# Optimization experiments

Measured on AMD Instinct MI355X. Metric: run time of the kernel, lower is better.

Reference implementation:

```python
import jax, jax.numpy as jnp
import numpy as np

B, S, F_IN, F_OUT = 8, 128, 768, 768
NUM_REL = 41           # num_dependencies + 1
NUM_LAYER = 2
N_HEAD, HID = 8, 96    # hidden_dim = embed_dim // n_head
EMB = 768


def setup_inputs() -> dict:
    key = jax.random.key(0)
    ks = jax.random.split(key, 14)
    s = 1.0 / np.sqrt(F_IN)
    inp = {
        "x": jax.random.normal(ks[0], (B, S, F_IN), dtype=jnp.float32),
        "adj": jax.random.uniform(ks[1], (B, NUM_REL, S, S), dtype=jnp.float32),
        "q": jax.random.normal(ks[2], (B, EMB), dtype=jnp.float32),
        # R-GCN params (stacked over layers)
        "w_rgcn": jax.random.uniform(ks[3], (NUM_LAYER, NUM_REL, F_IN, F_OUT), minval=-s, maxval=s),
        "score_w": jax.random.uniform(ks[4], (NUM_LAYER, F_OUT), minval=-s, maxval=s),
        "score_b": jax.random.uniform(ks[5], (NUM_LAYER,), minval=-s, maxval=s),
        # Attention params (stored as [in, out] for x @ W)
        "wk": jax.random.uniform(ks[6], (EMB, N_HEAD * HID), minval=-s, maxval=s),
        "bk": jnp.zeros((N_HEAD * HID,), jnp.float32),
        "wq": jax.random.uniform(ks[7], (EMB, N_HEAD * HID), minval=-s, maxval=s),
        "bq": jnp.zeros((N_HEAD * HID,), jnp.float32),
        "wbil": jax.random.uniform(ks[8], (HID, HID), minval=-1.0 / np.sqrt(HID), maxval=1.0 / np.sqrt(HID)),
        "wproj": jax.random.uniform(ks[9], (N_HEAD * HID, EMB), minval=-s, maxval=s),
        "bproj": jnp.zeros((EMB,), jnp.float32),
    }
    return inp


def _rgcn_layer(h, adj, w, sw, sb):
    # h: [B,S,I]; adj: [B,R,S,S]; w: [R,I,O]
    hidden = jnp.einsum("bsi,rio->brso", h, w)            # per-relation transform
    denom = jnp.sum(adj, axis=3, keepdims=True)           # [B,R,S,1]
    intm = jnp.einsum("brsk,brko->brso", adj, hidden)     # relation-wise aggregation
    div = intm / jnp.where(denom == 0, jnp.ones_like(denom), denom)
    logits = jnp.einsum("brso,o->brs", div, sw) + sb      # score Linear(out->1)
    r_coeffs = jax.nn.softmax(logits, axis=1)             # softmax over relations
    out = jnp.einsum("brso,brs->bso", div, r_coeffs)
    return jax.nn.relu(out)


def _attention(k, q, wk, bk, wq, bq, wbil, wproj, bproj):
    # k: [B,S,E]; q: [B,E] -> [B,1,E]
    q3 = q[:, None, :]
    kx = (k @ wk + bk).reshape(B, S, N_HEAD, HID)
    qx = (q3 @ wq + bq).reshape(B, 1, N_HEAD, HID)
    qw = jnp.einsum("bqhd,de->bqhe", qx, wbil)            # bi_linear score
    score = jnp.einsum("bqhe,bkhe->bhqk", qw, kx)
    attn = jax.nn.softmax(score, axis=-1)
    o = jnp.einsum("bhqk,bkhd->bqhd", attn, kx).reshape(B, 1, N_HEAD * HID)
    return o @ wproj + bproj                              # [B,1,EMB]


def reference(x, adj, q, w_rgcn, score_w, score_b, wk, bk, wq, bq, wbil, wproj, bproj):
    h = x
    for l in range(NUM_LAYER):
        h = _rgcn_layer(h, adj, w_rgcn[l], score_w[l], score_b[l])
    return _attention(h, q, wk, bk, wq, bq, wbil, wproj, bproj)
```

## Files before the change

kernel.cpp:

```cpp
#include <hip/hip_runtime.h>
#include <stdint.h>

#define B_ 8
#define S_ 128
#define R_ 41
#define F_ 768
#define NH_ 8
#define HID_ 96
#define BS_ (B_*S_)
#define SM_SCALE 256.0f
#define NG_ 21

typedef _Float16 f16;
typedef _Float16 f16x8 __attribute__((ext_vector_type(8)));
typedef _Float16 f16x4 __attribute__((ext_vector_type(4)));
typedef _Float16 f16x2 __attribute__((ext_vector_type(2)));
typedef float f32x4 __attribute__((ext_vector_type(4)));
typedef float f32x2 __attribute__((ext_vector_type(2)));

#define GLD16(gp, lp) __builtin_amdgcn_global_load_lds((const __attribute__((address_space(1))) uint32_t*)(gp), (__attribute__((address_space(3))) uint32_t*)(lp), 16, 0, 0)

__device__ __forceinline__ float wredsum(float v){
  #pragma unroll
  for (int o=32;o;o>>=1) v += __shfl_down(v,o,64);
  return v;
}

__global__ __launch_bounds__(256) void kConvWV(const float* __restrict__ w, const float* __restrict__ sw,
                                               f16* __restrict__ wT, float* __restrict__ v) {
  int bid = blockIdx.x;
  int it = bid % 12, r = bid / 12;
  __shared__ float t[64*68];
  int tid = threadIdx.x;
  int ri = tid >> 2, c = tid & 3;
  float vacc = 0.f;
  for (int ot = 0; ot < 12; ++ot) {
    const float* src = w + ((size_t)r*F_ + (it*64 + ri))*F_ + ot*64 + c*16;
    const float* swp = sw + ot*64 + c*16;
    __syncthreads();
    #pragma unroll
    for (int j=0;j<4;j++){
      f32x4 v4 = *(const f32x4*)(src + j*4);
      f32x4 s4 = *(const f32x4*)(swp + j*4);
      vacc += v4.x*s4.x + v4.y*s4.y + v4.z*s4.z + v4.w*s4.w;
      *(f32x4*)&t[ri*68 + c*16 + j*4] = v4;
    }
    __syncthreads();
    int ro = tid >> 2;
    f16 outv[16];
    #pragma unroll
    for (int j=0;j<16;j++) outv[j] = (f16)t[(c*16+j)*68 + ro];
    f16* dst = wT + ((size_t)r*F_ + (ot*64+ro))*F_ + it*64 + c*16;
    *(f16x8*)dst = *(f16x8*)&outv[0];
    *(f16x8*)(dst+8) = *(f16x8*)&outv[8];
  }
  vacc += __shfl_down(vacc, 1, 64);
  vacc += __shfl_down(vacc, 2, 64);
  if (c == 0) v[(size_t)r*F_ + it*64 + ri] = vacc;
}

__global__ __launch_bounds__(256) void kConvW(const float* __restrict__ w, f16* __restrict__ wT) {
  int bid = blockIdx.x;
  int ot = bid % 12; int it = (bid/12) % 12; int r = bid / 144;
  __shared__ float t[64*68];
  int tid = threadIdx.x;
  int ri = tid >> 2, c = tid & 3;
  const float* src = w + ((size_t)r*F_ + (it*64 + ri))*F_ + ot*64 + c*16;
  #pragma unroll
  for (int j=0;j<4;j++){
    f32x4 v4 = *(const f32x4*)(src + j*4);
    *(f32x4*)&t[ri*68 + c*16 + j*4] = v4;
  }
  __syncthreads();
  int ro = tid >> 2;
  f16 outv[16];
  #pragma unroll
  for (int j=0;j<16;j++) outv[j] = (f16)t[(c*16+j)*68 + ro];
  f16* dst = wT + ((size_t)r*F_ + (ot*64+ro))*F_ + it*64 + c*16;
  *(f16x8*)dst = *(f16x8*)&outv[0];
  *(f16x8*)(dst+8) = *(f16x8*)&outv[8];
}

template<typename T>
__global__ __launch_bounds__(256) void kTransTo16T(const T* __restrict__ h, f16* __restrict__ hT) {
  int bid = blockIdx.x;
  int st = bid & 1; int ft = (bid>>1) % 12; int b = bid / 24;
  __shared__ f16 t[64*72];
  int tid = threadIdx.x;
  int sl = tid>>2, c = tid&3;
  const T* src = h + ((size_t)b*S_ + st*64 + sl)*F_ + ft*64 + c*16;
  f16 tmp[16];
  #pragma unroll
  for (int j=0;j<16;j++) tmp[j] = (f16)src[j];
  *(f16x8*)&t[sl*72 + c*16]     = *(f16x8*)&tmp[0];
  *(f16x8*)&t[sl*72 + c*16 + 8] = *(f16x8*)&tmp[8];
  __syncthreads();
  int fl = tid>>2;
  f16 outv[16];
  #pragma unroll
  for (int j=0;j<16;j++) outv[j] = t[(c*16+j)*72 + fl];
  f16* dst = hT + ((size_t)b*F_ + ft*64 + fl)*S_ + st*64 + c*16;
  *(f16x8*)dst = *(f16x8*)&outv[0];
  *(f16x8*)(dst+8) = *(f16x8*)&outv[8];
}

__global__ __launch_bounds__(256) void kUL(const float* __restrict__ h, const float* __restrict__ v,
                    const float* __restrict__ adj, const float* __restrict__ sb_all, int l,
                    float* __restrict__ dinv, float* __restrict__ lg) {
  int bid = blockIdx.x;
  int r = bid % R_, b = bid / R_;
  __shared__ float v_s[F_];
  __shared__ float u_s[S_];
  int tid = threadIdx.x;
  #pragma unroll
  for (int j=0;j<3;j++) v_s[tid + j*256] = v[(size_t)r*F_ + tid + j*256];
  __syncthreads();
  int wid = tid>>6, lane = tid&63;
  for (int kl=0; kl<32; ++kl){
    int k = wid*32 + kl;
    const float* hr = h + ((size_t)b*S_ + k)*F_ + lane*12;
    const float* vp = &v_s[lane*12];
    float acc=0.f;
    #pragma unroll
    for (int j=0;j<3;j++){
      f32x4 a = *(const f32x4*)(hr+j*4);
      f32x4 c4 = *(const f32x4*)(vp+j*4);
      acc += a.x*c4.x+a.y*c4.y+a.z*c4.z+a.w*c4.w;
    }
    acc = wredsum(acc);
    if (lane==0) u_s[k] = acc;
  }
  __syncthreads();
  int s = tid>>1, half = tid&1;
  const float* arow = adj + ((size_t)bid*S_ + s)*S_ + half*64;
  const float* up = &u_s[half*64];
  float ssum=0.f, sdot=0.f;
  #pragma unroll
  for (int j=0;j<16;j++){
    f32x4 a = *(const f32x4*)(arow + j*4);
    ssum += a.x+a.y+a.z+a.w;
    sdot += a.x*up[j*4] + a.y*up[j*4+1] + a.z*up[j*4+2] + a.w*up[j*4+3];
  }
  ssum += __shfl_xor(ssum,1,64);
  sdot += __shfl_xor(sdot,1,64);
  if (half==0){
    float dv = (ssum==0.0f)?1.0f:(1.0f/ssum);
    dinv[(size_t)bid*S_ + s] = dv;
    lg[(size_t)bid*S_ + s] = sdot*dv + sb_all[l];
  }
}

__global__ __launch_bounds__(64) void kSM16(const float* __restrict__ lg, const float* __restrict__ dinv,
                     const float* __restrict__ adj, f16* __restrict__ M) {
  int bid = blockIdx.x;
  int b = bid >> 7, s = bid & 127;
  int lane = threadIdx.x;
  __shared__ float coef[R_];
  float x = (lane < R_) ? lg[((size_t)b*R_ + lane)*S_ + s] : -1e30f;
  float m = x;
  #pragma unroll
  for (int o=32;o;o>>=1) m = fmaxf(m, __shfl_xor(m,o,64));
  float e = (lane < R_) ? expf(x - m) : 0.f;
  float sum = e;
  #pragma unroll
  for (int o=32;o;o>>=1) sum += __shfl_xor(sum,o,64);
  if (lane < R_) coef[lane] = e/sum * SM_SCALE * dinv[((size_t)b*R_ + lane)*S_ + s];
  __syncthreads();
  for (int r=0;r<R_;r++){
    float cc = coef[r];
    size_t base = (((size_t)(b*R_+r))*S_ + s)*S_ + lane*2;
    f32x2 a2 = *(const f32x2*)(adj + base);
    f16x2 o2; o2[0]=(f16)(a2.x*cc); o2[1]=(f16)(a2.y*cc);
    *(f16x2*)(M + base) = o2;
  }
}

__global__ __launch_bounds__(256) void kGgemm(const f16* __restrict__ M, const f16* __restrict__ hT, f16* __restrict__ G) {
  __shared__ f16 lds[2*16384];
  f16* lsA = lds;
  f16* lsB = lds + 16384;
  int bid = blockIdx.x;
  int nt = bid % 6; int r = (bid/6) % R_; int b = bid/(6*R_);
  int tid = threadIdx.x, wid = tid>>6, lane = tid&63;
  const f16* Ab = M + (size_t)(b*R_ + r)*(S_*S_);
  const f16* Bb = hT + ((size_t)b*F_ + nt*128)*S_;
  #pragma unroll
  for (int j=0;j<8;j++){
    int qd = wid*8 + j;
    GLD16(Ab + qd*512 + lane*8, lsA + qd*512);
    GLD16(Bb + qd*512 + lane*8, lsB + qd*512);
  }
  __syncthreads();
  f32x4 acc[4][4] = {};
  int wr = wid>>1, wc = wid&1;
  int lr = lane&15, kk0 = (lane>>4)*8;
  #pragma unroll
  for (int ks=0;ks<4;ks++){
    int kk = ks*32 + kk0;
    f16x8 av[4], bv[4];
    #pragma unroll
    for (int i=0;i<4;i++) av[i] = *(const f16x8*)&lsA[(wr*64+i*16+lr)*128 + kk];
    #pragma unroll
    for (int i=0;i<4;i++) bv[i] = *(const f16x8*)&lsB[(wc*64+i*16+lr)*128 + kk];
    #pragma unroll
    for (int mi=0;mi<4;mi++)
      #pragma unroll
      for (int ni=0;ni<4;ni++)
        acc[mi][ni] = __builtin_amdgcn_mfma_f32_16x16x32_f16(av[mi],bv[ni],acc[mi][ni],0,0,0);
  }
  __syncthreads();
  #pragma unroll
  for (int mi=0;mi<4;mi++)
    #pragma unroll
    for (int ni=0;ni<4;ni++){
      int row = wr*64 + mi*16 + (lane>>4)*4;
      int col = wc*64 + ni*16 + lr;
      #pragma unroll
      for (int i=0;i<4;i++)
        lds[(row+i)*136 + col] = (f16)acc[mi][ni][i];
    }
  __syncthreads();
  int row = tid>>1, seg = tid&1;
  f16* dst = G + ((size_t)(b*R_ + r)*S_ + row)*F_ + nt*128 + seg*64;
  const f16* sl = lds + row*136 + seg*64;
  #pragma unroll
  for (int j=0;j<8;j++) *(f16x8*)(dst + j*8) = *(const f16x8*)(sl + j*8);
}

__global__ __launch_bounds__(512,2) void kOutGemm(const f16* __restrict__ G, const f16* __restrict__ WT, float* __restrict__ Cp) {
  __shared__ f16 ls[2][2][256*64];
  int bid = blockIdx.x;
  int t12 = bid % 12, g = bid / 12;
  int nt = t12 % 3, mt = t12 / 3;
  int r0 = (g<20)? 2*g : 40;
  int nr = (g<20)? 2 : 1;
  int tid = threadIdx.x, wid = tid>>6, lane = tid&63;
  size_t abase[4], bbase[4];
  #pragma unroll
  for (int j=0;j<4;j++){
    int chunk = wid*4 + j;
    int arow = mt*256 + chunk*8 + (lane>>3);
    int b = arow >> 7, s = arow & 127;
    abase[j] = ((size_t)b*R_*S_ + s)*(size_t)F_ + (lane&7)*8;
    int orow = nt*256 + chunk*8 + (lane>>3);
    bbase[j] = (size_t)orow*F_ + (lane&7)*8;
  }
  f32x4 acc[8][4] = {};
  int wr = wid>>2, wc = wid&3;
  int lr = lane&15, kk0 = (lane>>4)*8;
  int nsteps = nr*12;
  auto STAGE = [&](int bf, int step){
    int r = r0 + step/12, it = step%12;
    const f16* Ar = G  + (size_t)r*S_*F_;
    const f16* Br = WT + (size_t)r*F_*F_;
    #pragma unroll
    for (int j=0;j<4;j++){
      int chunk = wid*4 + j;
      GLD16(Ar + abase[j] + it*64, &ls[bf][0][chunk*512]);
      GLD16(Br + bbase[j] + it*64, &ls[bf][1][chunk*512]);
    }
  };
  STAGE(0, 0);
  __syncthreads();
  int cur = 0;
  for (int step=0; step<nsteps; ++step){
    if (step+1 < nsteps) STAGE(cur^1, step+1);
    __builtin_amdgcn_s_setprio(1);
    #pragma unroll
    for (int ks=0;ks<2;ks++){
      int kk = ks*32 + kk0;
      f16x8 av[8], bv[4];
      #pragma unroll
      for (int i=0;i<8;i++) av[i] = *(const f16x8*)&ls[cur][0][(wr*128+i*16+lr)*64 + kk];
      #pragma unroll
      for (int i=0;i<4;i++) bv[i] = *(const f16x8*)&ls[cur][1][(wc*64+i*16+lr)*64 + kk];
      #pragma unroll
      for (int mi=0;mi<8;mi++)
        #pragma unroll
        for (int ni=0;ni<4;ni++)
          acc[mi][ni] = __builtin_amdgcn_mfma_f32_16x16x32_f16(av[mi],bv[ni],acc[mi][ni],0,0,0);
    }
    __builtin_amdgcn_s_setprio(0);
    __syncthreads();
    cur ^= 1;
  }
  #pragma unroll
  for (int mi=0;mi<8;mi++)
    #pragma unroll
    for (int ni=0;ni<4;ni++){
      int row = mt*256 + wr*128 + mi*16 + (lane>>4)*4;
      int col = nt*256 + wc*64 + ni*16 + lr;
      #pragma unroll
      for (int i=0;i<4;i++)
        Cp[((size_t)g*BS_ + row + i)*F_ + col] = acc[mi][ni][i];
    }
}

__global__ __launch_bounds__(256) void kReduce(const float* __restrict__ Cp, float* __restrict__ h32, f16* __restrict__ h16o) {
  int t = blockIdx.x*256 + threadIdx.x;
  size_t i4 = (size_t)t*4;
  f32x4 s = {};
  #pragma unroll
  for (int g=0; g<NG_; g++){
    f32x4 v4 = *(const f32x4*)(Cp + (size_t)g*BS_*F_ + i4);
    s.x += v4.x; s.y += v4.y; s.z += v4.z; s.w += v4.w;
  }
  const float inv = 1.0f/SM_SCALE;
  f32x4 rr;
  rr.x = fmaxf(s.x*inv, 0.f); rr.y = fmaxf(s.y*inv, 0.f);
  rr.z = fmaxf(s.z*inv, 0.f); rr.w = fmaxf(s.w*inv, 0.f);
  *(f32x4*)(h32 + i4) = rr;
  f16x4 o; o[0]=(f16)rr.x; o[1]=(f16)rr.y; o[2]=(f16)rr.z; o[3]=(f16)rr.w;
  *(f16x4*)(h16o + i4) = o;
}

__global__ __launch_bounds__(256) void kKx(const f16* __restrict__ A, const f16* __restrict__ BT,
                    const float* __restrict__ bias, float* __restrict__ C) {
  __shared__ f16 ls[2][2][128*64];
  int bid = blockIdx.x;
  int nt = bid % 6, mt = bid / 6;
  int tid = threadIdx.x, wid = tid>>6, lane = tid&63;
  size_t abase[4], bbase[4];
  #pragma unroll
  for (int j=0;j<4;j++){
    int qd = wid*4 + j;
    int row = mt*128 + qd*8 + (lane>>3);
    abase[j] = (size_t)row*F_ + (lane&7)*8;
    int o = nt*128 + qd*8 + (lane>>3);
    bbase[j] = (size_t)o*F_ + (lane&7)*8;
  }
  f32x4 acc[4][4] = {};
  int wr = wid>>1, wc = wid&1;
  int lr = lane&15, kk0 = (lane>>4)*8;
  auto STAGE = [&](int bf, int it){
    #pragma unroll
    for (int j=0;j<4;j++){
      int qd = wid*4+j;
      GLD16(A + abase[j] + it*64, &ls[bf][0][qd*512]);
      GLD16(BT + bbase[j] + it*64, &ls[bf][1][qd*512]);
    }
  };
  STAGE(0, 0);
  __syncthreads();
  int cur = 0;
  for (int it=0; it<12; ++it){
    if (it+1 < 12) STAGE(cur^1, it+1);
    #pragma unroll
    for (int ks=0;ks<2;ks++){
      int kk = ks*32 + kk0;
      f16x8 av[4], bv[4];
      #pragma unroll
      for (int i=0;i<4;i++) av[i] = *(const f16x8*)&ls[cur][0][(wr*64+i*16+lr)*64 + kk];
      #pragma unroll
      for (int i=0;i<4;i++) bv[i] = *(const f16x8*)&ls[cur][1][(wc*64+i*16+lr)*64 + kk];
      #pragma unroll
      for (int mi=0;mi<4;mi++)
        #pragma unroll
        for (int ni=0;ni<4;ni++)
          acc[mi][ni] = __builtin_amdgcn_mfma_f32_16x16x32_f16(av[mi],bv[ni],acc[mi][ni],0,0,0);
    }
    __syncthreads();
    cur ^= 1;
  }
  #pragma unroll
  for (int mi=0;mi<4;mi++)
    #pragma unroll
    for (int ni=0;ni<4;ni++){
      int row = mt*128 + wr*64 + mi*16 + (lane>>4)*4;
      int col = nt*128 + wc*64 + ni*16 + lr;
      float bb = bias[col];
      #pragma unroll
      for (int i=0;i<4;i++)
        C[(size_t)(row+i)*F_ + col] = acc[mi][ni][i] + bb;
    }
}

__global__ __launch_bounds__(256) void kAttn(const float* __restrict__ kx, const float* __restrict__ qin,
                      const float* __restrict__ wq, const float* __restrict__ bq,
                      const float* __restrict__ wbil, float* __restrict__ obuf) {
  int bid = blockIdx.x; int h = bid & 7; int b = bid >> 3;
  __shared__ float qx[HID_], qw[HID_], sc[S_];
  __shared__ float smax, ssum;
  int t = threadIdx.x;
  if (t < HID_) {
    float a0=0.f,a1=0.f,a2=0.f,a3=0.f;
    const float* qp = qin + (size_t)b*F_;
    const float* wp = wq + h*HID_ + t;
    for (int i=0;i<F_;i+=4){
      a0 += qp[i]*wp[(size_t)i*F_];
      a1 += qp[i+1]*wp[(size_t)(i+1)*F_];
      a2 += qp[i+2]*wp[(size_t)(i+2)*F_];
      a3 += qp[i+3]*wp[(size_t)(i+3)*F_];
    }
    qx[t] = a0+a1+a2+a3 + bq[h*HID_+t];
  }
  __syncthreads();
  if (t < HID_) {
    float a0=0.f,a1=0.f;
    for (int e=0;e<HID_;e+=2){ a0 += qx[e]*wbil[e*HID_+t]; a1 += qx[e+1]*wbil[(e+1)*HID_+t]; }
    qw[t] = a0+a1;
  }
  __syncthreads();
  if (t < S_) {
    float a0=0.f,a1=0.f;
    const float* kp = kx + ((size_t)b*S_ + t)*F_ + h*HID_;
    for (int e=0;e<HID_;e+=2){ a0 += qw[e]*kp[e]; a1 += qw[e+1]*kp[e+1]; }
    sc[t] = a0+a1;
  }
  __syncthreads();
  if (t < 64) {
    float m = fmaxf(sc[t], sc[t+64]);
    #pragma unroll
    for (int o=32;o;o>>=1) m = fmaxf(m, __shfl_down(m,o,64));
    if (t==0) smax = m;
  }
  __syncthreads();
  if (t < S_) sc[t] = expf(sc[t]-smax);
  __syncthreads();
  if (t < 64) {
    float s = sc[t] + sc[t+64];
    s = wredsum(s);
    if (t==0) ssum = s;
  }
  __syncthreads();
  if (t < HID_) {
    float a0=0.f,a1=0.f;
    const float* kp = kx + ((size_t)b*S_)*F_ + h*HID_ + t;
    for (int k=0;k<S_;k+=2){ a0 += sc[k]*kp[(size_t)k*F_]; a1 += sc[k+1]*kp[(size_t)(k+1)*F_]; }
    obuf[(size_t)b*F_ + h*HID_ + t] = (a0+a1)/ssum;
  }
}

__global__ __launch_bounds__(256) void kProj(const float* __restrict__ obuf, const float* __restrict__ wproj,
                      const float* __restrict__ bproj, float* __restrict__ outp) {
  int bid = blockIdx.x; int b = bid/3, seg = bid%3;
  int t = threadIdx.x;
  __shared__ float ov[F_];
  for (int j=t;j<F_;j+=256) ov[j] = obuf[(size_t)b*F_ + j];
  __syncthreads();
  int col = seg*256 + t;
  float a0=0.f,a1=0.f,a2=0.f,a3=0.f;
  for (int j=0;j<F_;j+=4){
    a0 += ov[j]*wproj[(size_t)j*F_+col];
    a1 += ov[j+1]*wproj[(size_t)(j+1)*F_+col];
    a2 += ov[j+2]*wproj[(size_t)(j+2)*F_+col];
    a3 += ov[j+3]*wproj[(size_t)(j+3)*F_+col];
  }
  outp[(size_t)b*F_ + col] = bproj[col] + a0+a1+a2+a3;
}

extern "C" void kernel_launch(void* const* d_in, const int* in_sizes, int n_in,
                              void* d_out, int out_size, void* d_ws, size_t ws_size,
                              hipStream_t stream) {
  (void)in_sizes; (void)n_in; (void)out_size;
  const float* x      = (const float*)d_in[0];
  const float* adj    = (const float*)d_in[1];
  const float* qin    = (const float*)d_in[2];
  const float* w_rgcn = (const float*)d_in[3];
  const float* score_w= (const float*)d_in[4];
  const float* score_b= (const float*)d_in[5];
  const float* wk     = (const float*)d_in[6];
  const float* bk     = (const float*)d_in[7];
  const float* wq     = (const float*)d_in[8];
  const float* bq     = (const float*)d_in[9];
  const float* wbil   = (const float*)d_in[10];
  const float* wproj  = (const float*)d_in[11];
  const float* bproj  = (const float*)d_in[12];
  float* outp = (float*)d_out;

  char* p = (char*)d_ws;
  auto alloc = [&](size_t bytes)->char* {
    char* r = p; p += (bytes + 255) & ~(size_t)255; return r;
  };
  f16*   w16T  = (f16*)  alloc((size_t)R_*F_*F_*2);
  f16*   G16   = (f16*)  alloc((size_t)B_*R_*S_*F_*2);
  f16*   M16   = (f16*)  alloc((size_t)B_*R_*S_*S_*2);
  float* Cpart = (float*)alloc((size_t)NG_*BS_*F_*4);
  float* h32a  = (float*)alloc((size_t)BS_*F_*4);
  float* h32b  = (float*)alloc((size_t)BS_*F_*4);
  f16*   h16row= (f16*)  alloc((size_t)BS_*F_*2);
  f16*   h16T  = (f16*)  alloc((size_t)BS_*F_*2);
  float* kx    = (float*)alloc((size_t)BS_*F_*4);
  f16*   wkT   = (f16*)  alloc((size_t)F_*F_*2);
  float* vbuf  = (float*)alloc((size_t)R_*F_*4);
  float* dinv  = (float*)alloc((size_t)B_*R_*S_*4);
  float* lgb   = (float*)alloc((size_t)B_*R_*S_*4);
  float* obuf  = (float*)alloc((size_t)B_*F_*4);
  if ((size_t)(p - (char*)d_ws) > ws_size) return;

  const size_t WL = (size_t)R_*F_*F_;

  kConvWV<<<R_*12, 256, 0, stream>>>(w_rgcn, score_w, w16T, vbuf);
  kTransTo16T<float><<<192, 256, 0, stream>>>(x, h16T);
  kUL<<<B_*R_, 256, 0, stream>>>(x, vbuf, adj, score_b, 0, dinv, lgb);
  kSM16<<<B_*S_, 64, 0, stream>>>(lgb, dinv, adj, M16);
  kGgemm<<<B_*R_*6, 256, 0, stream>>>(M16, h16T, G16);
  kOutGemm<<<12*NG_, 512, 0, stream>>>(G16, w16T, Cpart);
  kReduce<<<768, 256, 0, stream>>>(Cpart, h32a, h16row);
  kTransTo16T<f16><<<192, 256, 0, stream>>>(h16row, h16T);

  kConvWV<<<R_*12, 256, 0, stream>>>(w_rgcn + WL, score_w + F_, w16T, vbuf);
  kUL<<<B_*R_, 256, 0, stream>>>(h32a, vbuf, adj, score_b, 1, dinv, lgb);
  kSM16<<<B_*S_, 64, 0, stream>>>(lgb, dinv, adj, M16);
  kGgemm<<<B_*R_*6, 256, 0, stream>>>(M16, h16T, G16);
  kOutGemm<<<12*NG_, 512, 0, stream>>>(G16, w16T, Cpart);
  kReduce<<<768, 256, 0, stream>>>(Cpart, h32b, h16row);

  kConvW<<<144, 256, 0, stream>>>(wk, wkT);
  kKx<<<48, 256, 0, stream>>>(h16row, wkT, bk, kx);
  kAttn<<<64, 256, 0, stream>>>(kx, qin, wq, bq, wbil, obuf);
  kProj<<<24, 256, 0, stream>>>(obuf, wproj, bproj, outp);
}
```

Before: 483.6 us.

## Swizzle LDS layouts in GEMMs and fuse reduce with transpose and weight conversion

Applies an XOR swizzle to the LDS tile layouts in kGgemm, kOutGemm and kKx so the MFMA operand reads avoid bank conflicts. It also fuses the partial-sum reduction with the f16 transpose into a new kReduceT kernel. The wk conversion is folded into the first kConvWV launch as extra blocks. Together these cut kernel launches and an extra pass over h, but the reduction now runs on 192 blocks instead of 768, which may lower memory parallelism. The final reduce also writes an unused transposed copy.

```diff
diff --git a/kernel.cpp b/kernel.cpp
--- a/kernel.cpp
+++ b/kernel.cpp
@@ -27,11 +27,33 @@
 }
 
 __global__ __launch_bounds__(256) void kConvWV(const float* __restrict__ w, const float* __restrict__ sw,
-                                               f16* __restrict__ wT, float* __restrict__ v) {
-  int bid = blockIdx.x;
+                                               f16* __restrict__ wT, float* __restrict__ v,
+                                               const float* __restrict__ wk, f16* __restrict__ wkT, int nwv) {
+  int bid = blockIdx.x;
+  int tid = threadIdx.x;
+  if (bid >= nwv) {
+    int b2 = bid - nwv;
+    int ot = b2 % 12; int it = b2 / 12;
+    __shared__ float t2[64*68];
+    int ri = tid >> 2, c = tid & 3;
+    const float* src = wk + (size_t)(it*64 + ri)*F_ + ot*64 + c*16;
+    #pragma unroll
+    for (int j=0;j<4;j++){
+      f32x4 v4 = *(const f32x4*)(src + j*4);
+      *(f32x4*)&t2[ri*68 + c*16 + j*4] = v4;
+    }
+    __syncthreads();
+    int ro = tid >> 2;
+    f16 outv[16];
+    #pragma unroll
+    for (int j=0;j<16;j++) outv[j] = (f16)t2[(c*16+j)*68 + ro];
+    f16* dst = wkT + (size_t)(ot*64+ro)*F_ + it*64 + c*16;
+    *(f16x8*)dst = *(f16x8*)&outv[0];
+    *(f16x8*)(dst+8) = *(f16x8*)&outv[8];
+    return;
+  }
   int it = bid % 12, r = bid / 12;
   __shared__ float t[64*68];
-  int tid = threadIdx.x;
   int ri = tid >> 2, c = tid & 3;
   float vacc = 0.f;
   for (int ot = 0; ot < 12; ++ot) {
@@ -59,36 +81,13 @@
   if (c == 0) v[(size_t)r*F_ + it*64 + ri] = vacc;
 }
 
-__global__ __launch_bounds__(256) void kConvW(const float* __restrict__ w, f16* __restrict__ wT) {
-  int bid = blockIdx.x;
-  int ot = bid % 12; int it = (bid/12) % 12; int r = bid / 144;
-  __shared__ float t[64*68];
-  int tid = threadIdx.x;
-  int ri = tid >> 2, c = tid & 3;
-  const float* src = w + ((size_t)r*F_ + (it*64 + ri))*F_ + ot*64 + c*16;
-  #pragma unroll
-  for (int j=0;j<4;j++){
-    f32x4 v4 = *(const f32x4*)(src + j*4);
-    *(f32x4*)&t[ri*68 + c*16 + j*4] = v4;
-  }
-  __syncthreads();
-  int ro = tid >> 2;
-  f16 outv[16];
-  #pragma unroll
-  for (int j=0;j<16;j++) outv[j] = (f16)t[(c*16+j)*68 + ro];
-  f16* dst = wT + ((size_t)r*F_ + (ot*64+ro))*F_ + it*64 + c*16;
-  *(f16x8*)dst = *(f16x8*)&outv[0];
-  *(f16x8*)(dst+8) = *(f16x8*)&outv[8];
-}
-
-template<typename T>
-__global__ __launch_bounds__(256) void kTransTo16T(const T* __restrict__ h, f16* __restrict__ hT) {
+__global__ __launch_bounds__(256) void kTransTo16T(const float* __restrict__ h, f16* __restrict__ hT) {
   int bid = blockIdx.x;
   int st = bid & 1; int ft = (bid>>1) % 12; int b = bid / 24;
   __shared__ f16 t[64*72];
   int tid = threadIdx.x;
   int sl = tid>>2, c = tid&3;
-  const T* src = h + ((size_t)b*S_ + st*64 + sl)*F_ + ft*64 + c*16;
+  const float* src = h + ((size_t)b*S_ + st*64 + sl)*F_ + ft*64 + c*16;
   f16 tmp[16];
   #pragma unroll
   for (int j=0;j<16;j++) tmp[j] = (f16)src[j];
@@ -187,21 +186,24 @@
   #pragma unroll
   for (int j=0;j<8;j++){
     int qd = wid*8 + j;
-    GLD16(Ab + qd*512 + lane*8, lsA + qd*512);
-    GLD16(Bb + qd*512 + lane*8, lsB + qd*512);
+    int rowg = qd*4 + (lane>>4);
+    int slotp = (lane&15) ^ ((j&3)*4 + (lane>>4));
+    GLD16(Ab + (size_t)rowg*128 + slotp*8, lsA + qd*512);
+    GLD16(Bb + (size_t)rowg*128 + slotp*8, lsB + qd*512);
   }
   __syncthreads();
   f32x4 acc[4][4] = {};
   int wr = wid>>1, wc = wid&1;
-  int lr = lane&15, kk0 = (lane>>4)*8;
+  int lr = lane&15, g4 = lane>>4;
   #pragma unroll
   for (int ks=0;ks<4;ks++){
-    int kk = ks*32 + kk0;
     f16x8 av[4], bv[4];
-    #pragma unroll
-    for (int i=0;i<4;i++) av[i] = *(const f16x8*)&lsA[(wr*64+i*16+lr)*128 + kk];
-    #pragma unroll
-    for (int i=0;i<4;i++) bv[i] = *(const f16x8*)&lsB[(wc*64+i*16+lr)*128 + kk];
+    int slotl = ks*4 + g4;
+    int slotp = slotl ^ lr;
+    #pragma unroll
+    for (int i=0;i<4;i++) av[i] = *(const f16x8*)&lsA[(wr*64+i*16+lr)*128 + slotp*8];
+    #pragma unroll
+    for (int i=0;i<4;i++) bv[i] = *(const f16x8*)&lsB[(wc*64+i*16+lr)*128 + slotp*8];
     #pragma unroll
     for (int mi=0;mi<4;mi++)
       #pragma unroll
@@ -235,19 +237,20 @@
   int r0 = (g<20)? 2*g : 40;
   int nr = (g<20)? 2 : 1;
   int tid = threadIdx.x, wid = tid>>6, lane = tid&63;
+  int swslot = (lane&7) ^ ((lane>>3)&7);
   size_t abase[4], bbase[4];
   #pragma unroll
   for (int j=0;j<4;j++){
     int chunk = wid*4 + j;
     int arow = mt*256 + chunk*8 + (lane>>3);
     int b = arow >> 7, s = arow & 127;
-    abase[j] = ((size_t)b*R_*S_ + s)*(size_t)F_ + (lane&7)*8;
+    abase[j] = ((size_t)b*R_*S_ + s)*(size_t)F_ + swslot*8;
     int orow = nt*256 + chunk*8 + (lane>>3);
-    bbase[j] = (size_t)orow*F_ + (lane&7)*8;
+    bbase[j] = (size_t)orow*F_ + swslot*8;
   }
   f32x4 acc[8][4] = {};
   int wr = wid>>2, wc = wid&3;
-  int lr = lane&15, kk0 = (lane>>4)*8;
+  int lr = lane&15, g4 = lane>>4, r7 = lane&7;
   int nsteps = nr*12;
   auto STAGE = [&](int bf, int step){
     int r = r0 + step/12, it = step%12;
@@ -268,12 +271,12 @@
     __builtin_amdgcn_s_setprio(1);
     #pragma unroll
     for (int ks=0;ks<2;ks++){
-      int kk = ks*32 + kk0;
+      int slotp = ((ks*4 + g4) ^ r7) * 8;
       f16x8 av[8], bv[4];
       #pragma unroll
-      for (int i=0;i<8;i++) av[i] = *(const f16x8*)&ls[cur][0][(wr*128+i*16+lr)*64 + kk];
-      #pragma unroll
-      for (int i=0;i<4;i++) bv[i] = *(const f16x8*)&ls[cur][1][(wc*64+i*16+lr)*64 + kk];
+      for (int i=0;i<8;i++) av[i] = *(const f16x8*)&ls[cur][0][(wr*128+i*16+lr)*64 + slotp];
+      #pragma unroll
+      for (int i=0;i<4;i++) bv[i] = *(const f16x8*)&ls[cur][1][(wc*64+i*16+lr)*64 + slotp];
       #pragma unroll
       for (int mi=0;mi<8;mi++)
         #pragma unroll
@@ -296,22 +299,42 @@
     }
 }
 
-__global__ __launch_bounds__(256) void kReduce(const float* __restrict__ Cp, float* __restrict__ h32, f16* __restrict__ h16o) {
-  int t = blockIdx.x*256 + threadIdx.x;
-  size_t i4 = (size_t)t*4;
-  f32x4 s = {};
-  #pragma unroll
-  for (int g=0; g<NG_; g++){
-    f32x4 v4 = *(const f32x4*)(Cp + (size_t)g*BS_*F_ + i4);
-    s.x += v4.x; s.y += v4.y; s.z += v4.z; s.w += v4.w;
-  }
+__global__ __launch_bounds__(256) void kReduceT(const float* __restrict__ Cp, float* __restrict__ h32,
+                                                f16* __restrict__ h16o, f16* __restrict__ hT) {
+  int bid = blockIdx.x;
+  int st = bid & 1; int ft = (bid>>1) % 12; int b = bid / 24;
+  __shared__ f16 t[64*72];
+  int tid = threadIdx.x;
+  int sl = tid>>2, c = tid&3;
+  size_t base = ((size_t)(b*S_ + st*64 + sl))*F_ + ft*64 + c*16;
   const float inv = 1.0f/SM_SCALE;
-  f32x4 rr;
-  rr.x = fmaxf(s.x*inv, 0.f); rr.y = fmaxf(s.y*inv, 0.f);
-  rr.z = fmaxf(s.z*inv, 0.f); rr.w = fmaxf(s.w*inv, 0.f);
-  *(f32x4*)(h32 + i4) = rr;
-  f16x4 o; o[0]=(f16)rr.x; o[1]=(f16)rr.y; o[2]=(f16)rr.z; o[3]=(f16)rr.w;
-  *(f16x4*)(h16o + i4) = o;
+  f16 tmp[16];
+  #pragma unroll
+  for (int q=0;q<4;q++){
+    f32x4 s4 = {};
+    #pragma unroll
+    for (int g=0; g<NG_; g++){
+      f32x4 v4 = *(const f32x4*)(Cp + (size_t)g*BS_*F_ + base + q*4);
+      s4.x += v4.x; s4.y += v4.y; s4.z += v4.z; s4.w += v4.w;
+    }
+    f32x4 rr;
+    rr.x = fmaxf(s4.x*inv, 0.f); rr.y = fmaxf(s4.y*inv, 0.f);
+    rr.z = fmaxf(s4.z*inv, 0.f); rr.w = fmaxf(s4.w*inv, 0.f);
+    *(f32x4*)(h32 + base + q*4) = rr;
+    tmp[q*4+0]=(f16)rr.x; tmp[q*4+1]=(f16)rr.y; tmp[q*4+2]=(f16)rr.z; tmp[q*4+3]=(f16)rr.w;
+  }
+  *(f16x8*)&t[sl*72 + c*16]     = *(f16x8*)&tmp[0];
+  *(f16x8*)&t[sl*72 + c*16 + 8] = *(f16x8*)&tmp[8];
+  *(f16x8*)(h16o + base)     = *(f16x8*)&tmp[0];
+  *(f16x8*)(h16o + base + 8) = *(f16x8*)&tmp[8];
+  __syncthreads();
+  int fl = tid>>2;
+  f16 outv[16];
+  #pragma unroll
+  for (int j=0;j<16;j++) outv[j] = t[(c*16+j)*72 + fl];
+  f16* dst = hT + ((size_t)b*F_ + ft*64 + fl)*S_ + st*64 + c*16;
+  *(f16x8*)dst = *(f16x8*)&outv[0];
+  *(f16x8*)(dst+8) = *(f16x8*)&outv[8];
 }
 
 __global__ __launch_bounds__(256) void kKx(const f16* __restrict__ A, const f16* __restrict__ BT,
@@ -320,18 +343,19 @@
   int bid = blockIdx.x;
   int nt = bid % 6, mt = bid / 6;
   int tid = threadIdx.x, wid = tid>>6, lane = tid&63;
+  int swslot = (lane&7) ^ ((lane>>3)&7);
   size_t abase[4], bbase[4];
   #pragma unroll
   for (int j=0;j<4;j++){
     int qd = wid*4 + j;
     int row = mt*128 + qd*8 + (lane>>3);
-    abase[j] = (size_t)row*F_ + (lane&7)*8;
+    abase[j] = (size_t)row*F_ + swslot*8;
     int o = nt*128 + qd*8 + (lane>>3);
-    bbase[j] = (size_t)o*F_ + (lane&7)*8;
+    bbase[j] = (size_t)o*F_ + swslot*8;
   }
   f32x4 acc[4][4] = {};
   int wr = wid>>1, wc = wid&1;
-  int lr = lane&15, kk0 = (lane>>4)*8;
+  int lr = lane&15, g4 = lane>>4, r7 = lane&7;
   auto STAGE = [&](int bf, int it){
     #pragma unroll
     for (int j=0;j<4;j++){
@@ -347,12 +371,12 @@
     if (it+1 < 12) STAGE(cur^1, it+1);
     #pragma unroll
     for (int ks=0;ks<2;ks++){
-      int kk = ks*32 + kk0;
+      int slotp = ((ks*4 + g4) ^ r7) * 8;
       f16x8 av[4], bv[4];
       #pragma unroll
-      for (int i=0;i<4;i++) av[i] = *(const f16x8*)&ls[cur][0][(wr*64+i*16+lr)*64 + kk];
-      #pragma unroll
-      for (int i=0;i<4;i++) bv[i] = *(const f16x8*)&ls[cur][1][(wc*64+i*16+lr)*64 + kk];
+      for (int i=0;i<4;i++) av[i] = *(const f16x8*)&ls[cur][0][(wr*64+i*16+lr)*64 + slotp];
+      #pragma unroll
+      for (int i=0;i<4;i++) bv[i] = *(const f16x8*)&ls[cur][1][(wc*64+i*16+lr)*64 + slotp];
       #pragma unroll
       for (int mi=0;mi<4;mi++)
         #pragma unroll
@@ -490,23 +514,21 @@
 
   const size_t WL = (size_t)R_*F_*F_;
 
-  kConvWV<<<R_*12, 256, 0, stream>>>(w_rgcn, score_w, w16T, vbuf);
-  kTransTo16T<float><<<192, 256, 0, stream>>>(x, h16T);
+  kConvWV<<<R_*12 + 144, 256, 0, stream>>>(w_rgcn, score_w, w16T, vbuf, wk, wkT, R_*12);
+  kTransTo16T<<<192, 256, 0, stream>>>(x, h16T);
   kUL<<<B_*R_, 256, 0, stream>>>(x, vbuf, adj, score_b, 0, dinv, lgb);
   kSM16<<<B_*S_, 64, 0, stream>>>(lgb, dinv, adj, M16);
   kGgemm<<<B_*R_*6, 256, 0, stream>>>(M16, h16T, G16);
   kOutGemm<<<12*NG_, 512, 0, stream>>>(G16, w16T, Cpart);
-  kReduce<<<768, 256, 0, stream>>>(Cpart, h32a, h16row);
-  kTransTo16T<f16><<<192, 256, 0, stream>>>(h16row, h16T);
-
-  kConvWV<<<R_*12, 256, 0, stream>>>(w_rgcn + WL, score_w + F_, w16T, vbuf);
+  kReduceT<<<192, 256, 0, stream>>>(Cpart, h32a, h16row, h16T);
+
+  kConvWV<<<R_*12, 256, 0, stream>>>(w_rgcn + WL, score_w + F_, w16T, vbuf, wk, wkT, R_*12);
   kUL<<<B_*R_, 256, 0, stream>>>(h32a, vbuf, adj, score_b, 1, dinv, lgb);
   kSM16<<<B_*S_, 64, 0, stream>>>(lgb, dinv, adj, M16);
   kGgemm<<<B_*R_*6, 256, 0, stream>>>(M16, h16T, G16);
   kOutGemm<<<12*NG_, 512, 0, stream>>>(G16, w16T, Cpart);
-  kReduce<<<768, 256, 0, stream>>>(Cpart, h32b, h16row);
-
-  kConvW<<<144, 256, 0, stream>>>(wk, wkT);
+  kReduceT<<<192, 256, 0, stream>>>(Cpart, h32b, h16row, h16T);
+
   kKx<<<48, 256, 0, stream>>>(h16row, wkT, bk, kx);
   kAttn<<<64, 256, 0, stream>>>(kx, qin, wq, bq, wbil, obuf);
   kProj<<<24, 256, 0, stream>>>(obuf, wproj, bproj, outp);
```

New measurement: 508.6 us. +5.2%, slower.
